# Optimization experiments

Hardware: AMD Instinct MI355X
Metric: run time of the kernel (lower is better)

The kernel has to match this reference:

```python
import jax, jax.numpy as jnp
import numpy as np

# DeepSeek-V3-style gate config
TOP_K = 8
N_EXPERTS = 256
N_GROUP = 8
TOPK_GROUP = 4
ROUTED_SCALING = 2.5
EPS = 1e-20


def setup_inputs() -> dict:
    key = jax.random.key(0)
    k1, k2, k3 = jax.random.split(key, 3)
    S, H = 16384, 7168
    hidden_states = jax.random.normal(k1, (S, H), dtype=jnp.float32)
    weight = jax.random.normal(k2, (N_EXPERTS, H), dtype=jnp.float32) * 0.02
    e_score_correction_bias = jax.random.normal(k3, (N_EXPERTS,), dtype=jnp.float32) * 0.1
    return {"hidden_states": hidden_states, "weight": weight,
            "e_score_correction_bias": e_score_correction_bias}


def reference(hidden_states, weight, e_score_correction_bias):
    S = hidden_states.shape[0]
    group_size = N_EXPERTS // N_GROUP  # 32

    # gating GEMM: [S, E]
    router_logits = jnp.einsum('sh,eh->se', hidden_states, weight)
    # scoring_func == 'sigmoid'
    scores = jax.nn.sigmoid(router_logits)
    scores_for_choice = scores + e_score_correction_bias[None, :]

    # group scores: sum of top-2 biased scores within each group -> [S, G]
    grouped = scores_for_choice.reshape(S, N_GROUP, group_size)
    top2_vals, _ = jax.lax.top_k(grouped, 2)
    group_scores = top2_vals.sum(axis=-1)

    # select top `TOPK_GROUP` groups, build group mask
    _, group_idx = jax.lax.top_k(group_scores, TOPK_GROUP)  # [S, topk_group]
    group_mask = jnp.zeros((S, N_GROUP), dtype=scores.dtype)
    group_mask = group_mask.at[jnp.arange(S)[:, None], group_idx].set(1.0)
    score_mask = jnp.repeat(group_mask, group_size, axis=-1)  # [S, E]

    # masked top-k over experts; weights gathered from UNBIASED scores
    tmp_scores = jnp.where(score_mask > 0, scores_for_choice, 0.0)
    _, topk_idx = jax.lax.top_k(tmp_scores, TOP_K)  # [S, top_k]
    topk_weight = jnp.take_along_axis(scores, topk_idx, axis=1)

    # renormalize (top_k > 1 and norm_topk_prob) then scale (noaux_tc)
    denom = topk_weight.sum(axis=-1, keepdims=True) + EPS
    topk_weight = topk_weight / denom * ROUTED_SCALING
    return topk_weight, topk_idx
```

## Files before the change

### kernel.cpp

```cpp
#include <hip/hip_runtime.h>
#include <math.h>

#define H_DIM 7168
#define N_EXP 256
#define N_GRP 8
#define G_SZ  32
#define TOPK_G 4
#define TOPK   8
#define BM 128
#define BK 32
#define S_TOK 16384
#define NTILES (H_DIM / BK)
#define NSPLIT 4
#define NQ     (NTILES / NSPLIT)
#define ITILES 2
#define NINT   (NQ / ITILES)
#define TILE_W_BYTES 32768
#define TILE_A_BYTES 16384

#define SA_SCALE 256.0f
#define SW_SCALE 4096.0f
#define DESCALE  (1.0f / 1048576.0f)

__device__ __align__(256) char g_wimg[(size_t)NTILES * TILE_W_BYTES];
__device__ __align__(256) float g_part[NSPLIT * (size_t)S_TOK * N_EXP];

typedef __attribute__((ext_vector_type(8))) _Float16 f16x8;
typedef __attribute__((ext_vector_type(4))) float f32x4;
typedef __attribute__((ext_vector_type(4))) unsigned short u16x4;
typedef __attribute__((ext_vector_type(8))) unsigned short u16x8;

__device__ inline void split2h(float x, unsigned short& h, unsigned short& l) {
    _Float16 hf = (_Float16)x;
    _Float16 lf = (_Float16)(x - (float)hf);
    h = __builtin_bit_cast(unsigned short, hf);
    l = __builtin_bit_cast(unsigned short, lf);
}

__global__ __launch_bounds__(256)
void convert_w_kernel(const float* __restrict__ W) {
    int idx  = blockIdx.x * 256 + threadIdx.x;
    int e    = idx / (H_DIM / 8);
    int koct = idx - e * (H_DIM / 8);
    int k0   = koct * 8;
    int t    = k0 >> 5;
    int o    = (k0 >> 3) & 3;
    int lane = (e & 15) | (o << 4);
    int eq   = e >> 6;
    int nj   = (e >> 4) & 3;
    const float* src = W + (size_t)e * H_DIM + k0;
    unsigned short h[8], l[8];
    #pragma unroll
    for (int j = 0; j < 8; ++j)
        split2h(src[j] * SW_SCALE, h[j], l[j]);
    char* base = g_wimg + (size_t)t * TILE_W_BYTES + (eq << 13) + (nj << 10) + (lane << 4);
    *(u16x8*)(base)        = u16x8{h[0],h[1],h[2],h[3],h[4],h[5],h[6],h[7]};
    *(u16x8*)(base + 4096) = u16x8{l[0],l[1],l[2],l[3],l[4],l[5],l[6],l[7]};
}

__global__ __launch_bounds__(512, 2)
void moe_gemm_quarter(const float* __restrict__ A)
{
    __shared__ __align__(128) char smem[2 * ITILES * TILE_A_BYTES];

    const int tid   = threadIdx.x;
    const int lane  = tid & 63;
    const int wave  = tid >> 6;
    const int mh    = wave >> 2;
    const int eq    = wave & 3;
    const int b     = blockIdx.x;
    const int kq    = b & 3;
    const int brow  = (b >> 2) * BM;

    const int fr    = lane & 15;
    const int fkb   = (lane >> 4) << 4;
    const int fswz  = ((fr << 6) + fkb) ^ ((fr & 7) << 4);
    const int abase = (mh << 12) + fswz;

    const int ar   = tid >> 3;
    const int akq  = tid & 7;
    const int aswz = ((ar << 6) + (akq << 3)) ^ ((ar & 7) << 4);
    const float4* Ag4 = reinterpret_cast<const float4*>(
        A + (size_t)(brow + ar) * H_DIM + kq * (H_DIM / NSPLIT)) + akq;
    const size_t ROW64 = (size_t)64 * (H_DIM / 4);

    f32x4 acc[4][4] = {};

    auto writeA2 = [&](const float4& v0, const float4& v1, char* ab) {
        unsigned short h0[4], l0[4], h1[4], l1[4];
        split2h(v0.x * SA_SCALE, h0[0], l0[0]); split2h(v0.y * SA_SCALE, h0[1], l0[1]);
        split2h(v0.z * SA_SCALE, h0[2], l0[2]); split2h(v0.w * SA_SCALE, h0[3], l0[3]);
        split2h(v1.x * SA_SCALE, h1[0], l1[0]); split2h(v1.y * SA_SCALE, h1[1], l1[1]);
        split2h(v1.z * SA_SCALE, h1[2], l1[2]); split2h(v1.w * SA_SCALE, h1[3], l1[3]);
        *(u16x4*)(ab + aswz)         = u16x4{h0[0], h0[1], h0[2], h0[3]};
        *(u16x4*)(ab + 4096 + aswz)  = u16x4{h1[0], h1[1], h1[2], h1[3]};
        *(u16x4*)(ab + 8192 + aswz)  = u16x4{l0[0], l0[1], l0[2], l0[3]};
        *(u16x4*)(ab + 12288 + aswz) = u16x4{l1[0], l1[1], l1[2], l1[3]};
    };

    const char* wsrc = g_wimg + (size_t)(kq * NQ) * TILE_W_BYTES
                       + (eq << 13) + (lane << 4);

    auto doTile = [&](int t, const char* ab) {
        const char* p = wsrc + (size_t)t * TILE_W_BYTES;
        f16x8 bh[4], bl[4];
        #pragma unroll
        for (int nj = 0; nj < 4; ++nj) {
            bh[nj] = *(const f16x8*)(p + (nj << 10));
            bl[nj] = *(const f16x8*)(p + 4096 + (nj << 10));
        }
        f16x8 ah[4];
        #pragma unroll
        for (int m = 0; m < 4; ++m)
            ah[m] = *(const f16x8*)(ab + abase + m * 1024);
        __builtin_amdgcn_s_setprio(1);
        #pragma unroll
        for (int nj = 0; nj < 4; ++nj)
            #pragma unroll
            for (int m = 0; m < 4; ++m)
                acc[m][nj] = __builtin_amdgcn_mfma_f32_16x16x32_f16(ah[m], bh[nj], acc[m][nj], 0, 0, 0);
        #pragma unroll
        for (int nj = 0; nj < 4; ++nj)
            #pragma unroll
            for (int m = 0; m < 4; ++m)
                acc[m][nj] = __builtin_amdgcn_mfma_f32_16x16x32_f16(ah[m], bl[nj], acc[m][nj], 0, 0, 0);
        __builtin_amdgcn_s_setprio(0);
        f16x8 al[4];
        #pragma unroll
        for (int m = 0; m < 4; ++m)
            al[m] = *(const f16x8*)(ab + 8192 + abase + m * 1024);
        __builtin_amdgcn_s_setprio(1);
        #pragma unroll
        for (int nj = 0; nj < 4; ++nj)
            #pragma unroll
            for (int m = 0; m < 4; ++m)
                acc[m][nj] = __builtin_amdgcn_mfma_f32_16x16x32_f16(al[m], bh[nj], acc[m][nj], 0, 0, 0);
        __builtin_amdgcn_s_setprio(0);
    };

    {
        float4 a00 = Ag4[0],      a01 = Ag4[ROW64];
        float4 a10 = Ag4[8],      a11 = Ag4[ROW64 + 8];
        writeA2(a00, a01, smem);
        writeA2(a10, a11, smem + TILE_A_BYTES);
        asm volatile("s_waitcnt lgkmcnt(0)" ::: "memory");
        __builtin_amdgcn_s_barrier();
    }

    #pragma unroll 1
    for (int i = 0; i < NINT; ++i) {
        char* cur = smem + (i & 1) * (ITILES * TILE_A_BYTES);
        char* nxt = smem + ((i + 1) & 1) * (ITILES * TILE_A_BYTES);
        const bool havenext = (i + 1 < NINT);
        const int ib = (havenext ? i + 1 : i) * ITILES;

        doTile(i * ITILES, cur);
        if (havenext) {
            float4 a00 = Ag4[(size_t)(ib + 0) * 8];
            float4 a01 = Ag4[ROW64 + (size_t)(ib + 0) * 8];
            float4 a10 = Ag4[(size_t)(ib + 1) * 8];
            float4 a11 = Ag4[ROW64 + (size_t)(ib + 1) * 8];
            writeA2(a00, a01, nxt);
            writeA2(a10, a11, nxt + TILE_A_BYTES);
        }
        doTile(i * ITILES + 1, cur + TILE_A_BYTES);
        asm volatile("s_waitcnt lgkmcnt(0)" ::: "memory");
        __builtin_amdgcn_s_barrier();
    }

    float* pb = g_part + ((size_t)kq * S_TOK + brow) * N_EXP;
    #pragma unroll
    for (int m = 0; m < 4; ++m)
        #pragma unroll
        for (int nj = 0; nj < 4; ++nj)
            #pragma unroll
            for (int q = 0; q < 4; ++q) {
                int row = (mh << 6) + m * 16 + ((lane >> 4) << 2) + q;
                int col = (eq << 6) + nj * 16 + (lane & 15);
                pb[row * N_EXP + col] = acc[m][nj][q];
            }
}

__global__ __launch_bounds__(256)
void gate_kernel(const float* __restrict__ bias, float* __restrict__ out, int S)
{
    const int lane = threadIdx.x & 63;
    const int row  = (blockIdx.x * 256 + threadIdx.x) >> 6;

    const float4 p0 = *(const float4*)(g_part + (size_t)row * N_EXP + lane * 4);
    const float4 p1 = *(const float4*)(g_part + ((size_t)S_TOK + row) * N_EXP + lane * 4);
    const float4 p2 = *(const float4*)(g_part + (2 * (size_t)S_TOK + row) * N_EXP + lane * 4);
    const float4 p3 = *(const float4*)(g_part + (3 * (size_t)S_TOK + row) * N_EXP + lane * 4);
    const float4 b4 = *(const float4*)(bias + lane * 4);

    float s[4], v[4];
    float m1 = -1e30f, m2 = -1e30f;
    {
        const float* q0 = (const float*)&p0;
        const float* q1 = (const float*)&p1;
        const float* q2 = (const float*)&p2;
        const float* q3 = (const float*)&p3;
        const float* qb = (const float*)&b4;
        #pragma unroll
        for (int j = 0; j < 4; ++j) {
            float x = (((q0[j] + q1[j]) + q2[j]) + q3[j]) * DESCALE;
            s[j] = 1.0f / (1.0f + expf(-x));
            float sb = s[j] + qb[j];
            v[j] = sb;
            if (sb > m1) { m2 = m1; m1 = sb; } else if (sb > m2) { m2 = sb; }
        }
    }
    #pragma unroll
    for (int d = 1; d < 8; d <<= 1) {
        float om1 = __shfl_xor(m1, d), om2 = __shfl_xor(m2, d);
        float hi = fmaxf(m1, om1), lo = fminf(m1, om1);
        m1 = hi;
        m2 = fmaxf(lo, fmaxf(m2, om2));
    }
    float gs = m1 + m2;
    float gsv[8];
    #pragma unroll
    for (int g = 0; g < 8; ++g) gsv[g] = __shfl(gs, g << 3);

    unsigned gmask = 0;
    #pragma unroll
    for (int t = 0; t < TOPK_G; ++t) {
        float best = -1e30f; int bg = 0;
        #pragma unroll
        for (int g = 0; g < 8; ++g) {
            bool avail = !((gmask >> g) & 1);
            if (avail && gsv[g] > best) { best = gsv[g]; bg = g; }
        }
        gmask |= 1u << bg;
    }

    const bool sel = (gmask >> (lane >> 3)) & 1;
    #pragma unroll
    for (int j = 0; j < 4; ++j) v[j] = sel ? v[j] : 0.0f;

    float wv[TOPK]; int wi[TOPK]; float wsum = 0.0f;
    #pragma unroll
    for (int t = 0; t < TOPK; ++t) {
        float bv = v[0]; int bj = 0;
        #pragma unroll
        for (int j = 1; j < 4; ++j)
            if (v[j] > bv) { bv = v[j]; bj = j; }
        int bidx = (lane << 2) | bj;
        #pragma unroll
        for (int d = 32; d >= 1; d >>= 1) {
            float ov = __shfl_xor(bv, d);
            int   oi = __shfl_xor(bidx, d);
            if (ov > bv || (ov == bv && oi < bidx)) { bv = ov; bidx = oi; }
        }
        int ol = bidx >> 2, oj = bidx & 3;
        float sl = s[0];
        if (oj == 1) sl = s[1]; else if (oj == 2) sl = s[2]; else if (oj == 3) sl = s[3];
        float sv = __shfl(sl, ol);
        wv[t] = sv; wi[t] = bidx; wsum += sv;
        if (lane == ol) {
            if (oj == 0) v[0] = -1e30f; else if (oj == 1) v[1] = -1e30f;
            else if (oj == 2) v[2] = -1e30f; else v[3] = -1e30f;
        }
    }

    if (lane == 0) {
        float scale = 2.5f / (wsum + 1e-20f);
        #pragma unroll
        for (int t = 0; t < TOPK; ++t) {
            out[(size_t)row * TOPK + t] = wv[t] * scale;
            out[(size_t)S * TOPK + (size_t)row * TOPK + t] = (float)wi[t];
        }
    }
}

extern "C" void kernel_launch(void* const* d_in, const int* in_sizes, int n_in,
                              void* d_out, int out_size, void* d_ws, size_t ws_size,
                              hipStream_t stream) {
    const float* A    = (const float*)d_in[0];
    const float* W    = (const float*)d_in[1];
    const float* bias = (const float*)d_in[2];
    float* out = (float*)d_out;
    const int S = in_sizes[0] / H_DIM;

    convert_w_kernel<<<dim3(N_EXP * (H_DIM / 8) / 256), 256, 0, stream>>>(W);
    moe_gemm_quarter<<<dim3(NSPLIT * S / BM), 512, 0, stream>>>(A);
    gate_kernel<<<dim3(S / 4), 256, 0, stream>>>(bias, out, S);
}
```

Measured before the change: 234.0 us.

## Halve GEMM block to 4 waves, each computing 128x64 per-wave tile

The split-K gating GEMM block shrinks from 8 waves (2 row halves × 4 expert quarters) to 4 waves, each covering all 128 rows for its 64 experts. Each wave reuses its loaded W fragments across twice as many rows, cutting global/L2 traffic for the weight image, and each thread now stages four float4s of A per tile instead of two. The cost is a doubled accumulator array (128 fp32 registers per lane), which raises register pressure, and fewer waves per block to hide latency.

Measured after the change: 219.8 us. 1.06x faster.

```diff
diff --git a/kernel.cpp b/kernel.cpp
--- a/kernel.cpp
+++ b/kernel.cpp
@@ -58,7 +58,7 @@
     *(u16x8*)(base + 4096) = u16x8{l[0],l[1],l[2],l[3],l[4],l[5],l[6],l[7]};
 }
 
-__global__ __launch_bounds__(512, 2)
+__global__ __launch_bounds__(256, 2)
 void moe_gemm_quarter(const float* __restrict__ A)
 {
     __shared__ __align__(128) char smem[2 * ITILES * TILE_A_BYTES];
@@ -66,8 +66,6 @@
     const int tid   = threadIdx.x;
     const int lane  = tid & 63;
     const int wave  = tid >> 6;
-    const int mh    = wave >> 2;
-    const int eq    = wave & 3;
     const int b     = blockIdx.x;
     const int kq    = b & 3;
     const int brow  = (b >> 2) * BM;
@@ -75,31 +73,28 @@
     const int fr    = lane & 15;
     const int fkb   = (lane >> 4) << 4;
     const int fswz  = ((fr << 6) + fkb) ^ ((fr & 7) << 4);
-    const int abase = (mh << 12) + fswz;
-
-    const int ar   = tid >> 3;
-    const int akq  = tid & 7;
-    const int aswz = ((ar << 6) + (akq << 3)) ^ ((ar & 7) << 4);
+
+    const int ar   = tid >> 1;
+    const int aq0  = (tid & 1) * 4;
     const float4* Ag4 = reinterpret_cast<const float4*>(
-        A + (size_t)(brow + ar) * H_DIM + kq * (H_DIM / NSPLIT)) + akq;
-    const size_t ROW64 = (size_t)64 * (H_DIM / 4);
-
-    f32x4 acc[4][4] = {};
-
-    auto writeA2 = [&](const float4& v0, const float4& v1, char* ab) {
-        unsigned short h0[4], l0[4], h1[4], l1[4];
-        split2h(v0.x * SA_SCALE, h0[0], l0[0]); split2h(v0.y * SA_SCALE, h0[1], l0[1]);
-        split2h(v0.z * SA_SCALE, h0[2], l0[2]); split2h(v0.w * SA_SCALE, h0[3], l0[3]);
-        split2h(v1.x * SA_SCALE, h1[0], l1[0]); split2h(v1.y * SA_SCALE, h1[1], l1[1]);
-        split2h(v1.z * SA_SCALE, h1[2], l1[2]); split2h(v1.w * SA_SCALE, h1[3], l1[3]);
-        *(u16x4*)(ab + aswz)         = u16x4{h0[0], h0[1], h0[2], h0[3]};
-        *(u16x4*)(ab + 4096 + aswz)  = u16x4{h1[0], h1[1], h1[2], h1[3]};
-        *(u16x4*)(ab + 8192 + aswz)  = u16x4{l0[0], l0[1], l0[2], l0[3]};
-        *(u16x4*)(ab + 12288 + aswz) = u16x4{l1[0], l1[1], l1[2], l1[3]};
+        A + (size_t)(brow + ar) * H_DIM + kq * (H_DIM / NSPLIT)) + aq0;
+
+    const char* wsrc = g_wimg + (size_t)(kq * NQ) * TILE_W_BYTES
+                       + (wave << 13) + (lane << 4);
+
+    f32x4 acc[8][4] = {};
+
+    auto writeA = [&](const float4* v, char* ab) {
+        #pragma unroll
+        for (int j = 0; j < 4; ++j) {
+            unsigned short h[4], l[4];
+            split2h(v[j].x * SA_SCALE, h[0], l[0]); split2h(v[j].y * SA_SCALE, h[1], l[1]);
+            split2h(v[j].z * SA_SCALE, h[2], l[2]); split2h(v[j].w * SA_SCALE, h[3], l[3]);
+            int off = ((ar << 6) + ((aq0 + j) << 3)) ^ ((ar & 7) << 4);
+            *(u16x4*)(ab + off)        = u16x4{h[0], h[1], h[2], h[3]};
+            *(u16x4*)(ab + 8192 + off) = u16x4{l[0], l[1], l[2], l[3]};
+        }
     };
-
-    const char* wsrc = g_wimg + (size_t)(kq * NQ) * TILE_W_BYTES
-                       + (eq << 13) + (lane << 4);
 
     auto doTile = [&](int t, const char* ab) {
         const char* p = wsrc + (size_t)t * TILE_W_BYTES;
@@ -109,40 +104,44 @@
             bh[nj] = *(const f16x8*)(p + (nj << 10));
             bl[nj] = *(const f16x8*)(p + 4096 + (nj << 10));
         }
-        f16x8 ah[4];
-        #pragma unroll
-        for (int m = 0; m < 4; ++m)
-            ah[m] = *(const f16x8*)(ab + abase + m * 1024);
-        __builtin_amdgcn_s_setprio(1);
-        #pragma unroll
-        for (int nj = 0; nj < 4; ++nj)
+        #pragma unroll
+        for (int mb = 0; mb < 2; ++mb) {
+            f16x8 ah[4];
             #pragma unroll
             for (int m = 0; m < 4; ++m)
-                acc[m][nj] = __builtin_amdgcn_mfma_f32_16x16x32_f16(ah[m], bh[nj], acc[m][nj], 0, 0, 0);
-        #pragma unroll
-        for (int nj = 0; nj < 4; ++nj)
+                ah[m] = *(const f16x8*)(ab + (mb * 4 + m) * 1024 + fswz);
+            __builtin_amdgcn_s_setprio(1);
+            #pragma unroll
+            for (int nj = 0; nj < 4; ++nj)
+                #pragma unroll
+                for (int m = 0; m < 4; ++m)
+                    acc[mb*4+m][nj] = __builtin_amdgcn_mfma_f32_16x16x32_f16(ah[m], bh[nj], acc[mb*4+m][nj], 0, 0, 0);
+            #pragma unroll
+            for (int nj = 0; nj < 4; ++nj)
+                #pragma unroll
+                for (int m = 0; m < 4; ++m)
+                    acc[mb*4+m][nj] = __builtin_amdgcn_mfma_f32_16x16x32_f16(ah[m], bl[nj], acc[mb*4+m][nj], 0, 0, 0);
+            __builtin_amdgcn_s_setprio(0);
+            f16x8 al[4];
             #pragma unroll
             for (int m = 0; m < 4; ++m)
-                acc[m][nj] = __builtin_amdgcn_mfma_f32_16x16x32_f16(ah[m], bl[nj], acc[m][nj], 0, 0, 0);
-        __builtin_amdgcn_s_setprio(0);
-        f16x8 al[4];
-        #pragma unroll
-        for (int m = 0; m < 4; ++m)
-            al[m] = *(const f16x8*)(ab + 8192 + abase + m * 1024);
-        __builtin_amdgcn_s_setprio(1);
-        #pragma unroll
-        for (int nj = 0; nj < 4; ++nj)
-            #pragma unroll
-            for (int m = 0; m < 4; ++m)
-                acc[m][nj] = __builtin_amdgcn_mfma_f32_16x16x32_f16(al[m], bh[nj], acc[m][nj], 0, 0, 0);
-        __builtin_amdgcn_s_setprio(0);
+                al[m] = *(const f16x8*)(ab + 8192 + (mb * 4 + m) * 1024 + fswz);
+            __builtin_amdgcn_s_setprio(1);
+            #pragma unroll
+            for (int nj = 0; nj < 4; ++nj)
+                #pragma unroll
+                for (int m = 0; m < 4; ++m)
+                    acc[mb*4+m][nj] = __builtin_amdgcn_mfma_f32_16x16x32_f16(al[m], bh[nj], acc[mb*4+m][nj], 0, 0, 0);
+            __builtin_amdgcn_s_setprio(0);
+        }
     };
 
     {
-        float4 a00 = Ag4[0],      a01 = Ag4[ROW64];
-        float4 a10 = Ag4[8],      a11 = Ag4[ROW64 + 8];
-        writeA2(a00, a01, smem);
-        writeA2(a10, a11, smem + TILE_A_BYTES);
+        float4 v0[4], v1[4];
+        #pragma unroll
+        for (int j = 0; j < 4; ++j) { v0[j] = Ag4[j]; v1[j] = Ag4[8 + j]; }
+        writeA(v0, smem);
+        writeA(v1, smem + TILE_A_BYTES);
         asm volatile("s_waitcnt lgkmcnt(0)" ::: "memory");
         __builtin_amdgcn_s_barrier();
     }
@@ -156,12 +155,14 @@
 
         doTile(i * ITILES, cur);
         if (havenext) {
-            float4 a00 = Ag4[(size_t)(ib + 0) * 8];
-            float4 a01 = Ag4[ROW64 + (size_t)(ib + 0) * 8];
-            float4 a10 = Ag4[(size_t)(ib + 1) * 8];
-            float4 a11 = Ag4[ROW64 + (size_t)(ib + 1) * 8];
-            writeA2(a00, a01, nxt);
-            writeA2(a10, a11, nxt + TILE_A_BYTES);
+            float4 v0[4], v1[4];
+            #pragma unroll
+            for (int j = 0; j < 4; ++j) {
+                v0[j] = Ag4[(size_t)(ib + 0) * 8 + j];
+                v1[j] = Ag4[(size_t)(ib + 1) * 8 + j];
+            }
+            writeA(v0, nxt);
+            writeA(v1, nxt + TILE_A_BYTES);
         }
         doTile(i * ITILES + 1, cur + TILE_A_BYTES);
         asm volatile("s_waitcnt lgkmcnt(0)" ::: "memory");
@@ -170,13 +171,13 @@
 
     float* pb = g_part + ((size_t)kq * S_TOK + brow) * N_EXP;
     #pragma unroll
-    for (int m = 0; m < 4; ++m)
+    for (int m = 0; m < 8; ++m)
         #pragma unroll
         for (int nj = 0; nj < 4; ++nj)
             #pragma unroll
             for (int q = 0; q < 4; ++q) {
-                int row = (mh << 6) + m * 16 + ((lane >> 4) << 2) + q;
-                int col = (eq << 6) + nj * 16 + (lane & 15);
+                int row = m * 16 + ((lane >> 4) << 2) + q;
+                int col = (wave << 6) + nj * 16 + (lane & 15);
                 pb[row * N_EXP + col] = acc[m][nj][q];
             }
 }
@@ -283,6 +284,6 @@
     const int S = in_sizes[0] / H_DIM;
 
     convert_w_kernel<<<dim3(N_EXP * (H_DIM / 8) / 256), 256, 0, stream>>>(W);
-    moe_gemm_quarter<<<dim3(NSPLIT * S / BM), 512, 0, stream>>>(A);
+    moe_gemm_quarter<<<dim3(NSPLIT * S / BM), 256, 0, stream>>>(A);
     gate_kernel<<<dim3(S / 4), 256, 0, stream>>>(bias, out, S);
 }
```
